# Kernel tuning notes

Hardware: AMD Instinct MI355X
Metric: run time of the kernel (lower is better)

Reference implementation:

```python
import jax, jax.numpy as jnp
import numpy as np

WINDOW = 5
PAD = (WINDOW - 1) // 2


def setup_inputs() -> dict:
    key = jax.random.key(0)
    k1, k2 = jax.random.split(key)
    pred = jax.random.uniform(k1, (8, 3, 512, 512), dtype=jnp.float32)
    gt = jax.random.uniform(k2, (8, 3, 512, 512), dtype=jnp.float32)
    return {"pred": pred, "gt": gt}


def reference(pred, gt):
    B, C, H, W = pred.shape
    # reflect-pad both images once
    pw = ((0, 0), (0, 0), (PAD, PAD), (PAD, PAD))
    pp = jnp.pad(pred, pw, mode="reflect")
    gp = jnp.pad(gt, pw, mode="reflect")
    p_ctr = pp[:, :, PAD:PAD + H, PAD:PAD + W]  # == pred
    g_ctr = gp[:, :, PAD:PAD + H, PAD:PAD + W]  # == gt
    # Fused: accumulate |census(pred) - census(gt)| per shifted compare,
    # never materializing the [B,C,H,W,window^2] census tensors.
    # (Original also cats a zeros plane first; it contributes 0 to the sum.)
    ham = jnp.zeros_like(pred)
    for i in range(WINDOW):
        for j in range(WINDOW):
            if i == PAD and j == PAD:
                continue
            p_cmp = (pp[:, :, i:i + H, j:j + W] < p_ctr).astype(pred.dtype)
            g_cmp = (gp[:, :, i:i + H, j:j + W] < g_ctr).astype(pred.dtype)
            ham = ham + jnp.abs(p_cmp - g_cmp)
    return jnp.mean(ham)
```

## Files before the change

### kernel.cpp

```cpp
#include <hip/hip_runtime.h>

#define IMG_H 512
#define IMG_W 512
#define N_IMG 24
#define NPIX (N_IMG * IMG_H * IMG_W)
#define ROWS_PT 4
#define NROWS 8
#define SLABS (IMG_H / ROWS_PT)
#define SCOLS (IMG_W / 4)
#define BLOCK 256
#define NBLOCKS ((N_IMG * SLABS * SCOLS) / BLOCK)

#define VMWAIT(N)                                             \
    asm volatile("s_waitcnt vmcnt(" #N ")" ::: "memory");     \
    __builtin_amdgcn_sched_barrier(0)

__device__ __forceinline__ int reflect_b(int x) {
    int a = x < 0 ? -x : x;
    int b = 2 * IMG_H - 2 - a;
    return a < b ? a : b;
}

__device__ __forceinline__ float4 gload4(const float* p) {
    float4 r;
    asm volatile("global_load_dwordx4 %0, %1, off" : "=v"(r) : "v"(p));
    return r;
}

__device__ __forceinline__ void fix_row(float4 A, float4 B, int w0, float w[8]) {
    const bool e0 = (w0 == 0);
    const bool e5 = (w0 == 508);
    w[0] = e0 ? A.z : A.x;
    w[1] = A.y;
    w[2] = e0 ? A.x : A.z;
    w[3] = e0 ? A.y : A.w;
    w[4] = e0 ? A.z : (e5 ? B.z : B.x);
    w[5] = e0 ? A.w : (e5 ? B.w : B.y);
    w[6] = B.z;
    w[7] = e5 ? B.y : B.w;
}

#define DO_ROW(R)                                                              \
    {                                                                          \
        const float pc0 = pw[(R) + 2][2], pc1 = pw[(R) + 2][3],                \
                    pc2 = pw[(R) + 2][4], pc3 = pw[(R) + 2][5];                \
        const float gc0 = gw[(R) + 2][2], gc1 = gw[(R) + 2][3],                \
                    gc2 = gw[(R) + 2][4], gc3 = gw[(R) + 2][5];                \
        _Pragma("unroll")                                                      \
        for (int dy = 0; dy < 5; ++dy) {                                       \
            const int row = (R) + dy;                                          \
            _Pragma("unroll")                                                  \
            for (int dx = 0; dx < 5; ++dx) {                                   \
                if (dy == 2 && dx == 2) continue;                              \
                c0 += (int)((pw[row][0 + dx] < pc0) != (gw[row][0 + dx] < gc0)); \
                c1 += (int)((pw[row][1 + dx] < pc1) != (gw[row][1 + dx] < gc1)); \
                c2 += (int)((pw[row][2 + dx] < pc2) != (gw[row][2 + dx] < gc2)); \
                c3 += (int)((pw[row][3 + dx] < pc3) != (gw[row][3 + dx] < gc3)); \
            }                                                                  \
        }                                                                      \
    }

__global__ __launch_bounds__(BLOCK, 2) void census_main(
    const float* __restrict__ pred, const float* __restrict__ gt,
    unsigned int* __restrict__ ws)
{
    const int t    = blockIdx.x * BLOCK + threadIdx.x;
    const int sc   = t & (SCOLS - 1);
    const int rest = t >> 7;
    const int slab = rest & (SLABS - 1);
    const int img  = rest >> 7;
    const int w0   = sc * 4;
    const int h0   = slab * ROWS_PT;

    const float* __restrict__ pimg = pred + (size_t)img * IMG_H * IMG_W;
    const float* __restrict__ gimg = gt   + (size_t)img * IMG_H * IMG_W;

    const int aL = max(0, min(w0 - 2, IMG_W - 6));
    const int aR = max(2, min(w0 + 2, IMG_W - 4));

    float4 pA[NROWS], pB[NROWS], gA[NROWS], gB[NROWS];
    #pragma unroll
    for (int i = 0; i < NROWS; ++i) {
        const int ry = reflect_b(h0 - 2 + i);
        const float* prow = pimg + ry * IMG_W;
        const float* grow = gimg + ry * IMG_W;
        pA[i] = gload4(prow + aL);
        pB[i] = gload4(prow + aR);
        gA[i] = gload4(grow + aL);
        gB[i] = gload4(grow + aR);
    }
    __builtin_amdgcn_sched_barrier(0);

    float pw[NROWS][8], gw[NROWS][8];
    int c0 = 0, c1 = 0, c2 = 0, c3 = 0;

    VMWAIT(24);
    fix_row(pA[0], pB[0], w0, pw[0]); fix_row(gA[0], gB[0], w0, gw[0]);
    fix_row(pA[1], pB[1], w0, pw[1]); fix_row(gA[1], gB[1], w0, gw[1]);

    VMWAIT(12);
    fix_row(pA[2], pB[2], w0, pw[2]); fix_row(gA[2], gB[2], w0, gw[2]);
    fix_row(pA[3], pB[3], w0, pw[3]); fix_row(gA[3], gB[3], w0, gw[3]);
    fix_row(pA[4], pB[4], w0, pw[4]); fix_row(gA[4], gB[4], w0, gw[4]);
    DO_ROW(0)

    VMWAIT(8);
    fix_row(pA[5], pB[5], w0, pw[5]); fix_row(gA[5], gB[5], w0, gw[5]);
    DO_ROW(1)

    VMWAIT(4);
    fix_row(pA[6], pB[6], w0, pw[6]); fix_row(gA[6], gB[6], w0, gw[6]);
    DO_ROW(2)

    VMWAIT(0);
    fix_row(pA[7], pB[7], w0, pw[7]); fix_row(gA[7], gB[7], w0, gw[7]);
    DO_ROW(3)

    int cnt = (c0 + c1) + (c2 + c3);

    #pragma unroll
    for (int off = 32; off > 0; off >>= 1)
        cnt += __shfl_down(cnt, off, 64);

    __shared__ int wave_sums[BLOCK / 64];
    const int lane = threadIdx.x & 63;
    const int wid  = threadIdx.x >> 6;
    if (lane == 0) wave_sums[wid] = cnt;
    __syncthreads();

    if (threadIdx.x == 0) {
        ws[blockIdx.x] = (unsigned int)(wave_sums[0] + wave_sums[1] +
                                        wave_sums[2] + wave_sums[3]);
    }
}

__global__ __launch_bounds__(BLOCK, 1) void census_reduce(
    const unsigned int* __restrict__ ws, float* __restrict__ out)
{
    unsigned int s = 0;
    #pragma unroll
    for (int i = 0; i < NBLOCKS / BLOCK; ++i)
        s += ws[threadIdx.x + i * BLOCK];

    #pragma unroll
    for (int off = 32; off > 0; off >>= 1)
        s += __shfl_down(s, off, 64);

    __shared__ unsigned int wsum[BLOCK / 64];
    const int lane = threadIdx.x & 63;
    const int wid  = threadIdx.x >> 6;
    if (lane == 0) wsum[wid] = s;
    __syncthreads();

    if (threadIdx.x == 0) {
        unsigned int tot = wsum[0] + wsum[1] + wsum[2] + wsum[3];
        out[0] = (float)((double)tot / (double)NPIX);
    }
}

extern "C" void kernel_launch(void* const* d_in, const int* in_sizes, int n_in,
                              void* d_out, int out_size, void* d_ws, size_t ws_size,
                              hipStream_t stream) {
    const float* pred = (const float*)d_in[0];
    const float* gt   = (const float*)d_in[1];
    float* out        = (float*)d_out;
    unsigned int* ws  = (unsigned int*)d_ws;

    census_main<<<NBLOCKS, BLOCK, 0, stream>>>(pred, gt, ws);
    census_reduce<<<1, BLOCK, 0, stream>>>(ws, out);
}
```

Baseline: 96.97 us.

## Stage row slabs in LDS with reflect halo instead of per-thread global loads

Each block now cooperatively loads an 8-row slab plus a 2-row halo for both images into shared memory, with reflected edge columns filled separately. Each thread then reads its 8x8 windows from LDS rather than issuing overlapping global loads. This removes redundant global traffic, since neighbouring threads previously re-fetched the same columns and rows, and it also drops the per-thread edge fixup. In exchange it adds a block-wide barrier, about 50KB of LDS per block (which caps occupancy), and a block-index swizzle across images, with launch bounds raised to 3 blocks.

```diff
diff --git a/kernel.cpp b/kernel.cpp
--- a/kernel.cpp
+++ b/kernel.cpp
@@ -4,16 +4,12 @@
 #define IMG_W 512
 #define N_IMG 24
 #define NPIX (N_IMG * IMG_H * IMG_W)
-#define ROWS_PT 4
-#define NROWS 8
-#define SLABS (IMG_H / ROWS_PT)
-#define SCOLS (IMG_W / 4)
+#define ROWS_PB 8
+#define SROWS 12
+#define LDSW 520
+#define RBLK (IMG_H / ROWS_PB)
 #define BLOCK 256
-#define NBLOCKS ((N_IMG * SLABS * SCOLS) / BLOCK)
-
-#define VMWAIT(N)                                             \
-    asm volatile("s_waitcnt vmcnt(" #N ")" ::: "memory");     \
-    __builtin_amdgcn_sched_barrier(0)
+#define NBLOCKS (N_IMG * RBLK)
 
 __device__ __forceinline__ int reflect_b(int x) {
     int a = x < 0 ? -x : x;
@@ -21,24 +17,18 @@
     return a < b ? a : b;
 }
 
-__device__ __forceinline__ float4 gload4(const float* p) {
-    float4 r;
-    asm volatile("global_load_dwordx4 %0, %1, off" : "=v"(r) : "v"(p));
-    return r;
-}
-
-__device__ __forceinline__ void fix_row(float4 A, float4 B, int w0, float w[8]) {
-    const bool e0 = (w0 == 0);
-    const bool e5 = (w0 == 508);
-    w[0] = e0 ? A.z : A.x;
-    w[1] = A.y;
-    w[2] = e0 ? A.x : A.z;
-    w[3] = e0 ? A.y : A.w;
-    w[4] = e0 ? A.z : (e5 ? B.z : B.x);
-    w[5] = e0 ? A.w : (e5 ? B.w : B.y);
-    w[6] = B.z;
-    w[7] = e5 ? B.y : B.w;
-}
+#define ROW_LD(K)                                                      \
+    {                                                                  \
+        const int r_ = sl4 + (K);                                      \
+        const float4 a_ = *(const float4*)&lds[0][r_][c4];             \
+        const float4 b_ = *(const float4*)&lds[0][r_][c4 + 4];         \
+        pw[K][0] = a_.x; pw[K][1] = a_.y; pw[K][2] = a_.z; pw[K][3] = a_.w; \
+        pw[K][4] = b_.x; pw[K][5] = b_.y; pw[K][6] = b_.z; pw[K][7] = b_.w; \
+        const float4 c_ = *(const float4*)&lds[1][r_][c4];             \
+        const float4 d_ = *(const float4*)&lds[1][r_][c4 + 4];         \
+        gw[K][0] = c_.x; gw[K][1] = c_.y; gw[K][2] = c_.z; gw[K][3] = c_.w; \
+        gw[K][4] = d_.x; gw[K][5] = d_.y; gw[K][6] = d_.z; gw[K][7] = d_.w; \
+    }
 
 #define DO_ROW(R)                                                              \
     {                                                                          \
@@ -60,61 +50,62 @@
         }                                                                      \
     }
 
-__global__ __launch_bounds__(BLOCK, 2) void census_main(
+__global__ __launch_bounds__(BLOCK, 3) void census_main(
     const float* __restrict__ pred, const float* __restrict__ gt,
     unsigned int* __restrict__ ws)
 {
-    const int t    = blockIdx.x * BLOCK + threadIdx.x;
-    const int sc   = t & (SCOLS - 1);
-    const int rest = t >> 7;
-    const int slab = rest & (SLABS - 1);
-    const int img  = rest >> 7;
-    const int w0   = sc * 4;
-    const int h0   = slab * ROWS_PT;
+    const int b   = blockIdx.x;
+    const int n   = (b & 7) * (NBLOCKS / 8) + (b >> 3);
+    const int img = n >> 6;
+    const int rb  = n & (RBLK - 1);
+    const int h0  = rb * ROWS_PB;
 
     const float* __restrict__ pimg = pred + (size_t)img * IMG_H * IMG_W;
     const float* __restrict__ gimg = gt   + (size_t)img * IMG_H * IMG_W;
 
-    const int aL = max(0, min(w0 - 2, IMG_W - 6));
-    const int aR = max(2, min(w0 + 2, IMG_W - 4));
+    __shared__ float lds[2][SROWS][LDSW];
 
-    float4 pA[NROWS], pB[NROWS], gA[NROWS], gB[NROWS];
-    #pragma unroll
-    for (int i = 0; i < NROWS; ++i) {
-        const int ry = reflect_b(h0 - 2 + i);
-        const float* prow = pimg + ry * IMG_W;
-        const float* grow = gimg + ry * IMG_W;
-        pA[i] = gload4(prow + aL);
-        pB[i] = gload4(prow + aR);
-        gA[i] = gload4(grow + aL);
-        gB[i] = gload4(grow + aR);
+    {
+        const int q  = threadIdx.x & 127;
+        const int rg = threadIdx.x >> 7;
+        #pragma unroll
+        for (int i = 0; i < 6; ++i) {
+            const int lr = rg + 2 * i;
+            const int gy = reflect_b(h0 - 2 + lr);
+            const float4 pv = *(const float4*)(pimg + (size_t)gy * IMG_W + 4 * q);
+            const float4 gv = *(const float4*)(gimg + (size_t)gy * IMG_W + 4 * q);
+            *(float2*)&lds[0][lr][2 + 4 * q] = make_float2(pv.x, pv.y);
+            *(float2*)&lds[0][lr][4 + 4 * q] = make_float2(pv.z, pv.w);
+            *(float2*)&lds[1][lr][2 + 4 * q] = make_float2(gv.x, gv.y);
+            *(float2*)&lds[1][lr][4 + 4 * q] = make_float2(gv.z, gv.w);
+        }
     }
-    __builtin_amdgcn_sched_barrier(0);
 
-    float pw[NROWS][8], gw[NROWS][8];
+    if (threadIdx.x < 96) {
+        const int r = threadIdx.x >> 3;
+        const int i = (threadIdx.x >> 2) & 1;
+        const int c = threadIdx.x & 3;
+        const int srccol = (c == 0) ? 2 : (c == 1) ? 1 : (c == 2) ? 510 : 509;
+        const int dst    = (c == 0) ? 0 : (c == 1) ? 1 : (c == 2) ? 514 : 515;
+        const int gy = reflect_b(h0 - 2 + r);
+        const float* base = i ? gimg : pimg;
+        lds[i][r][dst] = base[(size_t)gy * IMG_W + srccol];
+    }
+    __syncthreads();
+
+    const int sc  = threadIdx.x & 127;
+    const int sl  = threadIdx.x >> 7;
+    const int c4  = 4 * sc;
+    const int sl4 = 4 * sl;
+
+    float pw[8][8], gw[8][8];
     int c0 = 0, c1 = 0, c2 = 0, c3 = 0;
 
-    VMWAIT(24);
-    fix_row(pA[0], pB[0], w0, pw[0]); fix_row(gA[0], gB[0], w0, gw[0]);
-    fix_row(pA[1], pB[1], w0, pw[1]); fix_row(gA[1], gB[1], w0, gw[1]);
-
-    VMWAIT(12);
-    fix_row(pA[2], pB[2], w0, pw[2]); fix_row(gA[2], gB[2], w0, gw[2]);
-    fix_row(pA[3], pB[3], w0, pw[3]); fix_row(gA[3], gB[3], w0, gw[3]);
-    fix_row(pA[4], pB[4], w0, pw[4]); fix_row(gA[4], gB[4], w0, gw[4]);
+    ROW_LD(0) ROW_LD(1) ROW_LD(2) ROW_LD(3) ROW_LD(4)
     DO_ROW(0)
-
-    VMWAIT(8);
-    fix_row(pA[5], pB[5], w0, pw[5]); fix_row(gA[5], gB[5], w0, gw[5]);
-    DO_ROW(1)
-
-    VMWAIT(4);
-    fix_row(pA[6], pB[6], w0, pw[6]); fix_row(gA[6], gB[6], w0, gw[6]);
-    DO_ROW(2)
-
-    VMWAIT(0);
-    fix_row(pA[7], pB[7], w0, pw[7]); fix_row(gA[7], gB[7], w0, gw[7]);
-    DO_ROW(3)
+    ROW_LD(5) DO_ROW(1)
+    ROW_LD(6) DO_ROW(2)
+    ROW_LD(7) DO_ROW(3)
 
     int cnt = (c0 + c1) + (c2 + c3);
 
```

Measured after the change: 96.43 us. About the same (-0.6%).
